# Performance work log

Measured on AMD Instinct MI355X. Metric: run time of the kernel, lower is better.

The kernel has to match this reference:

```python
import jax, jax.numpy as jnp
import numpy as np

NEG_BIG = -9e15  # matches torch's -9000000000000000.0 mask value
ALPHA = 0.2      # LeakyReLU negative slope


def setup_inputs() -> dict:
    key = jax.random.key(0)
    k1, k2, k3 = jax.random.split(key, 3)
    B, N, Fin, Fout = 8, 2048, 64, 64
    h = jax.random.normal(k1, (B, N, Fin), dtype=jnp.float32)
    adj = jax.random.randint(k2, (B, N, N), 0, 2, dtype=jnp.int32)
    kW, ka = jax.random.split(k3)
    # xavier_uniform with gain=1.414
    gW = 1.414 * np.sqrt(6.0 / (Fin + Fout))
    W = jax.random.uniform(kW, (Fin, Fout), minval=-gW, maxval=gW, dtype=jnp.float32)
    ga = 1.414 * np.sqrt(6.0 / (2 * Fout + 1))
    a = jax.random.uniform(ka, (2 * Fout, 1), minval=-ga, maxval=ga, dtype=jnp.float32)
    return {"h": h, "adj": adj, "W": W, "a": a}


def reference(h, adj, W, a):
    # Wh: [B, N, Fout]
    Wh = jnp.einsum("bnf,fo->bno", h, W)
    Fout = W.shape[1]
    a1 = a[:Fout, 0]   # source part of attention vector
    a2 = a[Fout:, 0]   # target part
    # e_ij = leakyrelu(a1.Wh_i + a2.Wh_j) -- rank-1 decomposition of the
    # repeat/cat construction; avoids the [B,N,N,2F] intermediate.
    s = Wh @ a1        # [B, N]
    t = Wh @ a2        # [B, N]
    e = s[:, :, None] + t[:, None, :]            # [B, N, N]
    e = jnp.where(e > 0, e, ALPHA * e)           # LeakyReLU
    e = jnp.where(adj > 0, e, NEG_BIG)           # adjacency mask
    attention = jax.nn.softmax(e, axis=2)
    # dropout omitted: reference is eval-mode (F.dropout is identity when not training)
    h_prime = jnp.einsum("bij,bjo->bio", attention, Wh)
    return jax.nn.elu(h_prime)                   # concat=True branch
```

## Files before the change

kernel.cpp:

```cpp
#include <hip/hip_runtime.h>


#define ALPHA 0.2f

typedef __attribute__((ext_vector_type(8))) short  short8;
typedef __attribute__((ext_vector_type(4))) float  f32x4;

static __device__ __forceinline__ unsigned short f2bf(float f) {
    unsigned u = __builtin_bit_cast(unsigned, f);
    u += 0x7fffu + ((u >> 16) & 1u);
    return (unsigned short)(u >> 16);
}

static __device__ __forceinline__ unsigned pack_bf2(float lo, float hi) {
    unsigned ulo = __builtin_bit_cast(unsigned, lo) + 0x8000u;
    unsigned uhi = __builtin_bit_cast(unsigned, hi) + 0x8000u;
    return __builtin_amdgcn_perm(uhi, ulo, 0x07060302);
}

__global__ __launch_bounds__(256) void k01(
    const float* __restrict__ h, const int* __restrict__ adj,
    const float* __restrict__ W, const float* __restrict__ a,
    unsigned short* __restrict__ whT, float* __restrict__ sw,
    float* __restrict__ tw, unsigned* __restrict__ mask)
{
    __shared__ float W_l[64 * 65];
    __shared__ float wa[128];
    __shared__ float tile[4 * 16 * 65];

    const int tid = threadIdx.x;

    if (blockIdx.x >= 256) {
        const int mb = blockIdx.x - 256;
        const int4* a4 = (const int4*)adj;
        #pragma unroll 1
        for (int batch = 0; batch < 4; ++batch) {
            const size_t base = (size_t)mb * 8192 + batch * 2048 + tid;
            int4 v[8];
            #pragma unroll
            for (int it = 0; it < 8; ++it) v[it] = a4[base + it * 256];
            #pragma unroll
            for (int it = 0; it < 8; ++it) {
                unsigned nib = (v[it].x != 0 ? 1u : 0u) | (v[it].y != 0 ? 2u : 0u)
                             | (v[it].z != 0 ? 4u : 0u) | (v[it].w != 0 ? 8u : 0u);
                unsigned w = nib << ((tid & 7) * 4);
                w |= __shfl_xor(w, 1, 64);
                w |= __shfl_xor(w, 2, 64);
                w |= __shfl_xor(w, 4, 64);
                if ((tid & 7) == 0) mask[(base + it * 256) >> 3] = w;
            }
        }
        return;
    }

    const int lane = tid & 63, wv = tid >> 6;
    const int im   = lane & 15, kq = lane >> 4;

    #pragma unroll
    for (int k = 0; k < 16; ++k) {
        int e = tid + 256 * k;
        W_l[(e >> 6) * 65 + (e & 63)] = W[e];
    }
    __syncthreads();

    if (tid < 128) {
        int f = tid & 63;
        const float* ap = a + (tid >> 6) * 64;
        float acc = 0.f;
        #pragma unroll 8
        for (int o = 0; o < 64; ++o) acc += W_l[f * 65 + o] * ap[o];
        wa[tid] = acc;
    }
    __syncthreads();

    short8 bf[4][2];
    #pragma unroll
    for (int nb = 0; nb < 4; ++nb)
        #pragma unroll
        for (int ks = 0; ks < 2; ++ks)
            #pragma unroll
            for (int u = 0; u < 8; ++u)
                bf[nb][ks][u] = (short)f2bf(W_l[(ks * 32 + kq * 8 + u) * 65 + nb * 16 + im]);

    const int row0 = blockIdx.x * 64 + wv * 16;
    const int bb = row0 >> 11, n_base = row0 & 2047;
    const float* hrow = h + (size_t)(row0 + im) * 64;

    float hv[2][8];
    short8 af[2];
    float sp = 0.f, tp = 0.f;
    #pragma unroll
    for (int ks = 0; ks < 2; ++ks) {
        float4 A = *(const float4*)(hrow + ks * 32 + kq * 8);
        float4 Bv = *(const float4*)(hrow + ks * 32 + kq * 8 + 4);
        hv[ks][0] = A.x;  hv[ks][1] = A.y;  hv[ks][2] = A.z;  hv[ks][3] = A.w;
        hv[ks][4] = Bv.x; hv[ks][5] = Bv.y; hv[ks][6] = Bv.z; hv[ks][7] = Bv.w;
        #pragma unroll
        for (int u = 0; u < 8; ++u) {
            int f = ks * 32 + kq * 8 + u;
            sp += hv[ks][u] * wa[f];
            tp += hv[ks][u] * wa[64 + f];
            af[ks][u] = (short)f2bf(hv[ks][u]);
        }
    }
    sp += __shfl_xor(sp, 16, 64); sp += __shfl_xor(sp, 32, 64);
    tp += __shfl_xor(tp, 16, 64); tp += __shfl_xor(tp, 32, 64);
    if (lane < 16) {
        sw[row0 + lane] = sp;
        tw[row0 + lane] = tp;
    }

    f32x4 acc[4] = {{0.f,0.f,0.f,0.f},{0.f,0.f,0.f,0.f},{0.f,0.f,0.f,0.f},{0.f,0.f,0.f,0.f}};
    #pragma unroll
    for (int ks = 0; ks < 2; ++ks)
        #pragma unroll
        for (int nb = 0; nb < 4; ++nb)
            acc[nb] = __builtin_amdgcn_mfma_f32_16x16x32_bf16(af[ks], bf[nb][ks], acc[nb], 0, 0, 0);

    #pragma unroll
    for (int nb = 0; nb < 4; ++nb)
        #pragma unroll
        for (int r = 0; r < 4; ++r)
            tile[wv * 1040 + (kq * 4 + r) * 65 + nb * 16 + im] = acc[nb][r];
    __syncthreads();

    #pragma unroll
    for (int k = 0; k < 16; ++k) {
        int o = kq + 4 * k;
        float v = tile[wv * 1040 + im * 65 + o];
        whT[(size_t)(bb * 64 + o) * 2048 + n_base + im] = f2bf(v);
    }
}

__global__ __launch_bounds__(256, 4) void k2_attn(
    const unsigned* __restrict__ mask, const unsigned short* __restrict__ whT,
    const float* __restrict__ sw, const float* __restrict__ tw,
    float* __restrict__ out)
{
    __shared__ float t_l[2048];
    __shared__ float cpart[4 * 1040];
    __shared__ float zp[64];

    const int tid  = threadIdx.x;
    const int lane = tid & 63, wv = tid >> 6;
    const int im   = lane & 15, kq = lane >> 4;
    const int b    = blockIdx.x >> 7;
    const int i0   = (blockIdx.x & 127) << 4;

    {
        const float4* tp4 = (const float4*)(tw + (size_t)b * 2048);
        *(float4*)&t_l[tid * 4]         = tp4[tid];
        *(float4*)&t_l[(tid + 256) * 4] = tp4[tid + 256];
    }

    const unsigned* mrow = mask + (size_t)(b * 2048 + i0 + im) * 64 + wv * 16;
    uint4 m0 = *(const uint4*)mrow,        m1 = *(const uint4*)(mrow + 4);
    uint4 m2 = *(const uint4*)(mrow + 8),  m3 = *(const uint4*)(mrow + 12);
    unsigned mm[16] = {m0.x, m0.y, m0.z, m0.w, m1.x, m1.y, m1.z, m1.w,
                       m2.x, m2.y, m2.z, m2.w, m3.x, m3.y, m3.z, m3.w};

    const float sl = sw[b * 2048 + i0 + im];
    const int j00 = wv * 512 + kq * 8;
    const unsigned short* whp0 = whT + ((size_t)(b * 64 +  0 + im) * 2048 + j00);
    const unsigned short* whp1 = whT + ((size_t)(b * 64 + 16 + im) * 2048 + j00);
    const unsigned short* whp2 = whT + ((size_t)(b * 64 + 32 + im) * 2048 + j00);
    const unsigned short* whp3 = whT + ((size_t)(b * 64 + 48 + im) * 2048 + j00);
    const int tbase = wv * 512 + kq * 8;

    __syncthreads();

    f32x4 acc0 = {0.f,0.f,0.f,0.f}, acc1 = {0.f,0.f,0.f,0.f};
    f32x4 acc2 = {0.f,0.f,0.f,0.f}, acc3 = {0.f,0.f,0.f,0.f};
    float zs = 0.f;

    short8 w0 = *(const short8*)(const void*)whp0;
    short8 w1 = *(const short8*)(const void*)whp1;
    short8 w2 = *(const short8*)(const void*)whp2;
    short8 w3 = *(const short8*)(const void*)whp3;

    #pragma unroll
    for (int s = 0; s < 16; ++s) {
        short8 n0 = w0, n1 = w1, n2 = w2, n3 = w3;
        if (s < 15) {
            n0 = *(const short8*)(const void*)(whp0 + (s + 1) * 32);
            n1 = *(const short8*)(const void*)(whp1 + (s + 1) * 32);
            n2 = *(const short8*)(const void*)(whp2 + (s + 1) * 32);
            n3 = *(const short8*)(const void*)(whp3 + (s + 1) * 32);
        }

        float4 tA = *(const float4*)&t_l[tbase + s * 32];
        float4 tB = *(const float4*)&t_l[tbase + s * 32 + 4];
        const unsigned mbyte = (mm[s] >> (kq * 8)) & 0xffu;

        float tv[8] = {tA.x, tA.y, tA.z, tA.w, tB.x, tB.y, tB.z, tB.w};
        float p[8];
        #pragma unroll
        for (int u = 0; u < 8; ++u) {
            float e = sl + tv[u];
            e = fmaxf(e, ALPHA * e);
            float w = __expf(e);
            p[u] = (mbyte & (1u << u)) ? w : 0.f;
            zs += p[u];
        }

        int4 ai;
        ai.x = (int)pack_bf2(p[0], p[1]);
        ai.y = (int)pack_bf2(p[2], p[3]);
        ai.z = (int)pack_bf2(p[4], p[5]);
        ai.w = (int)pack_bf2(p[6], p[7]);
        short8 af = __builtin_bit_cast(short8, ai);

        acc0 = __builtin_amdgcn_mfma_f32_16x16x32_bf16(af, w0, acc0, 0, 0, 0);
        acc1 = __builtin_amdgcn_mfma_f32_16x16x32_bf16(af, w1, acc1, 0, 0, 0);
        acc2 = __builtin_amdgcn_mfma_f32_16x16x32_bf16(af, w2, acc2, 0, 0, 0);
        acc3 = __builtin_amdgcn_mfma_f32_16x16x32_bf16(af, w3, acc3, 0, 0, 0);

        w0 = n0; w1 = n1; w2 = n2; w3 = n3;
    }

    zs += __shfl_xor(zs, 16, 64);
    zs += __shfl_xor(zs, 32, 64);
    if (lane < 16) zp[wv * 16 + lane] = zs;

    #pragma unroll
    for (int r = 0; r < 4; ++r) {
        cpart[wv * 1040 + (kq * 4 + r) * 65 +  0 + im] = acc0[r];
        cpart[wv * 1040 + (kq * 4 + r) * 65 + 16 + im] = acc1[r];
        cpart[wv * 1040 + (kq * 4 + r) * 65 + 32 + im] = acc2[r];
        cpart[wv * 1040 + (kq * 4 + r) * 65 + 48 + im] = acc3[r];
    }
    __syncthreads();

    #pragma unroll
    for (int k = 0; k < 4; ++k) {
        int idx = tid + 256 * k;
        int i = idx >> 6, o = idx & 63;
        float ssum = cpart[0 * 1040 + i * 65 + o] + cpart[1 * 1040 + i * 65 + o]
                   + cpart[2 * 1040 + i * 65 + o] + cpart[3 * 1040 + i * 65 + o];
        float z = zp[i] + zp[16 + i] + zp[32 + i] + zp[48 + i];
        if (z == 0.f) z = 1.f;
        float r = ssum / z;
        out[((size_t)(b * 2048 + i0 + i)) * 64 + o] = r > 0.f ? r : expm1f(r);
    }
}

extern "C" void kernel_launch(void* const* d_in, const int* in_sizes, int n_in,
                              void* d_out, int out_size, void* d_ws, size_t ws_size,
                              hipStream_t stream) {
    const float* h   = (const float*)d_in[0];
    const int*   adj = (const int*)d_in[1];
    const float* W   = (const float*)d_in[2];
    const float* a   = (const float*)d_in[3];
    float* out = (float*)d_out;

    unsigned short* whT = (unsigned short*)d_ws;
    float* sw  = (float*)((char*)d_ws + 2097152);
    float* tw  = (float*)((char*)d_ws + 2097152 + 65536);
    unsigned* mask = (unsigned*)((char*)d_ws + 2097152 + 131072);

    hipLaunchKernelGGL(k01, dim3(1280), dim3(256), 0, stream, h, adj, W, a, whT, sw, tw, mask);
    hipLaunchKernelGGL(k2_attn, dim3(1024), dim3(256), 0, stream, mask, whT, sw, tw, out);
}
```

Before: 236.1 us.

## Pack adjacency mask per-thread to bytes, drop prefetch, relax k2 launch bounds

The adjacency-to-bitmask pass now has each thread read two int4 vectors and write one mask byte directly. This removes the cross-lane shuffle reduction and the strided word stores. The attention kernel drops its manual software prefetch of the Wh tiles and loads them inside the unrolled loop, leaving scheduling to the compiler. Launch bounds change from 4 to 2 waves per SIMD, which gives more registers but may lower occupancy. The exp calls are made conditional on the mask bit and the row-sum accumulation is written as a reduction tree.

```diff
diff --git a/kernel.cpp b/kernel.cpp
--- a/kernel.cpp
+++ b/kernel.cpp
@@ -22,7 +22,7 @@
     const float* __restrict__ h, const int* __restrict__ adj,
     const float* __restrict__ W, const float* __restrict__ a,
     unsigned short* __restrict__ whT, float* __restrict__ sw,
-    float* __restrict__ tw, unsigned* __restrict__ mask)
+    float* __restrict__ tw, unsigned char* __restrict__ mask)
 {
     __shared__ float W_l[64 * 65];
     __shared__ float wa[128];
@@ -34,21 +34,25 @@
         const int mb = blockIdx.x - 256;
         const int4* a4 = (const int4*)adj;
         #pragma unroll 1
-        for (int batch = 0; batch < 4; ++batch) {
-            const size_t base = (size_t)mb * 8192 + batch * 2048 + tid;
-            int4 v[8];
-            #pragma unroll
-            for (int it = 0; it < 8; ++it) v[it] = a4[base + it * 256];
-            #pragma unroll
-            for (int it = 0; it < 8; ++it) {
-                unsigned nib = (v[it].x != 0 ? 1u : 0u) | (v[it].y != 0 ? 2u : 0u)
-                             | (v[it].z != 0 ? 4u : 0u) | (v[it].w != 0 ? 8u : 0u);
-                unsigned w = nib << ((tid & 7) * 4);
-                w |= __shfl_xor(w, 1, 64);
-                w |= __shfl_xor(w, 2, 64);
-                w |= __shfl_xor(w, 4, 64);
-                if ((tid & 7) == 0) mask[(base + it * 256) >> 3] = w;
-            }
+        for (int g0 = 0; g0 < 16; g0 += 4) {
+            int4 v0a, v0b, v1a, v1b, v2a, v2b, v3a, v3b;
+            const size_t p0 = (size_t)mb * 4096 + (size_t)g0 * 256 + tid;
+            v0a = a4[p0 * 2];          v0b = a4[p0 * 2 + 1];
+            v1a = a4[(p0 + 256) * 2];  v1b = a4[(p0 + 256) * 2 + 1];
+            v2a = a4[(p0 + 512) * 2];  v2b = a4[(p0 + 512) * 2 + 1];
+            v3a = a4[(p0 + 768) * 2];  v3b = a4[(p0 + 768) * 2 + 1];
+            unsigned b0 = (v0a.x ? 1u:0u)|(v0a.y ? 2u:0u)|(v0a.z ? 4u:0u)|(v0a.w ? 8u:0u)
+                        | (v0b.x ?16u:0u)|(v0b.y ?32u:0u)|(v0b.z ?64u:0u)|(v0b.w ?128u:0u);
+            unsigned b1 = (v1a.x ? 1u:0u)|(v1a.y ? 2u:0u)|(v1a.z ? 4u:0u)|(v1a.w ? 8u:0u)
+                        | (v1b.x ?16u:0u)|(v1b.y ?32u:0u)|(v1b.z ?64u:0u)|(v1b.w ?128u:0u);
+            unsigned b2 = (v2a.x ? 1u:0u)|(v2a.y ? 2u:0u)|(v2a.z ? 4u:0u)|(v2a.w ? 8u:0u)
+                        | (v2b.x ?16u:0u)|(v2b.y ?32u:0u)|(v2b.z ?64u:0u)|(v2b.w ?128u:0u);
+            unsigned b3 = (v3a.x ? 1u:0u)|(v3a.y ? 2u:0u)|(v3a.z ? 4u:0u)|(v3a.w ? 8u:0u)
+                        | (v3b.x ?16u:0u)|(v3b.y ?32u:0u)|(v3b.z ?64u:0u)|(v3b.w ?128u:0u);
+            mask[p0]       = (unsigned char)b0;
+            mask[p0 + 256] = (unsigned char)b1;
+            mask[p0 + 512] = (unsigned char)b2;
+            mask[p0 + 768] = (unsigned char)b3;
         }
         return;
     }
@@ -132,7 +136,7 @@
     }
 }
 
-__global__ __launch_bounds__(256, 4) void k2_attn(
+__global__ __launch_bounds__(256, 2) void k2_attn(
     const unsigned* __restrict__ mask, const unsigned short* __restrict__ whT,
     const float* __restrict__ sw, const float* __restrict__ tw,
     float* __restrict__ out)
@@ -153,11 +157,10 @@
         *(float4*)&t_l[(tid + 256) * 4] = tp4[tid + 256];
     }
 
-    const unsigned* mrow = mask + (size_t)(b * 2048 + i0 + im) * 64 + wv * 16;
-    uint4 m0 = *(const uint4*)mrow,        m1 = *(const uint4*)(mrow + 4);
-    uint4 m2 = *(const uint4*)(mrow + 8),  m3 = *(const uint4*)(mrow + 12);
-    unsigned mm[16] = {m0.x, m0.y, m0.z, m0.w, m1.x, m1.y, m1.z, m1.w,
-                       m2.x, m2.y, m2.z, m2.w, m3.x, m3.y, m3.z, m3.w};
+    const uint4* mrow4 = (const uint4*)(mask + (size_t)(b * 2048 + i0 + im) * 64 + wv * 16);
+    const uint4 mA = mrow4[0], mB = mrow4[1], mC = mrow4[2], mD = mrow4[3];
+    const unsigned mm[16] = {mA.x, mA.y, mA.z, mA.w, mB.x, mB.y, mB.z, mB.w,
+                             mC.x, mC.y, mC.z, mC.w, mD.x, mD.y, mD.z, mD.w};
 
     const float sl = sw[b * 2048 + i0 + im];
     const int j00 = wv * 512 + kq * 8;
@@ -165,7 +168,6 @@
     const unsigned short* whp1 = whT + ((size_t)(b * 64 + 16 + im) * 2048 + j00);
     const unsigned short* whp2 = whT + ((size_t)(b * 64 + 32 + im) * 2048 + j00);
     const unsigned short* whp3 = whT + ((size_t)(b * 64 + 48 + im) * 2048 + j00);
-    const int tbase = wv * 512 + kq * 8;
 
     __syncthreads();
 
@@ -173,49 +175,48 @@
     f32x4 acc2 = {0.f,0.f,0.f,0.f}, acc3 = {0.f,0.f,0.f,0.f};
     float zs = 0.f;
 
-    short8 w0 = *(const short8*)(const void*)whp0;
-    short8 w1 = *(const short8*)(const void*)whp1;
-    short8 w2 = *(const short8*)(const void*)whp2;
-    short8 w3 = *(const short8*)(const void*)whp3;
-
     #pragma unroll
     for (int s = 0; s < 16; ++s) {
-        short8 n0 = w0, n1 = w1, n2 = w2, n3 = w3;
-        if (s < 15) {
-            n0 = *(const short8*)(const void*)(whp0 + (s + 1) * 32);
-            n1 = *(const short8*)(const void*)(whp1 + (s + 1) * 32);
-            n2 = *(const short8*)(const void*)(whp2 + (s + 1) * 32);
-            n3 = *(const short8*)(const void*)(whp3 + (s + 1) * 32);
-        }
-
-        float4 tA = *(const float4*)&t_l[tbase + s * 32];
-        float4 tB = *(const float4*)&t_l[tbase + s * 32 + 4];
+        const short8 w0 = *(const short8*)(const void*)(whp0 + s * 32);
+        const short8 w1 = *(const short8*)(const void*)(whp1 + s * 32);
+        const short8 w2 = *(const short8*)(const void*)(whp2 + s * 32);
+        const short8 w3 = *(const short8*)(const void*)(whp3 + s * 32);
+
+        const float4 tA = *(const float4*)&t_l[j00 + s * 32];
+        const float4 tB = *(const float4*)&t_l[j00 + s * 32 + 4];
         const unsigned mbyte = (mm[s] >> (kq * 8)) & 0xffu;
 
-        float tv[8] = {tA.x, tA.y, tA.z, tA.w, tB.x, tB.y, tB.z, tB.w};
-        float p[8];
-        #pragma unroll
-        for (int u = 0; u < 8; ++u) {
-            float e = sl + tv[u];
-            e = fmaxf(e, ALPHA * e);
-            float w = __expf(e);
-            p[u] = (mbyte & (1u << u)) ? w : 0.f;
-            zs += p[u];
-        }
+        float e0 = sl + tA.x; e0 = fmaxf(e0, ALPHA * e0);
+        float e1 = sl + tA.y; e1 = fmaxf(e1, ALPHA * e1);
+        float e2 = sl + tA.z; e2 = fmaxf(e2, ALPHA * e2);
+        float e3 = sl + tA.w; e3 = fmaxf(e3, ALPHA * e3);
+        float e4 = sl + tB.x; e4 = fmaxf(e4, ALPHA * e4);
+        float e5 = sl + tB.y; e5 = fmaxf(e5, ALPHA * e5);
+        float e6 = sl + tB.z; e6 = fmaxf(e6, ALPHA * e6);
+        float e7 = sl + tB.w; e7 = fmaxf(e7, ALPHA * e7);
+
+        float p0 = (mbyte &   1u) ? __expf(e0) : 0.f;
+        float p1 = (mbyte &   2u) ? __expf(e1) : 0.f;
+        float p2 = (mbyte &   4u) ? __expf(e2) : 0.f;
+        float p3 = (mbyte &   8u) ? __expf(e3) : 0.f;
+        float p4 = (mbyte &  16u) ? __expf(e4) : 0.f;
+        float p5 = (mbyte &  32u) ? __expf(e5) : 0.f;
+        float p6 = (mbyte &  64u) ? __expf(e6) : 0.f;
+        float p7 = (mbyte & 128u) ? __expf(e7) : 0.f;
+
+        zs += ((p0 + p1) + (p2 + p3)) + ((p4 + p5) + (p6 + p7));
 
         int4 ai;
-        ai.x = (int)pack_bf2(p[0], p[1]);
-        ai.y = (int)pack_bf2(p[2], p[3]);
-        ai.z = (int)pack_bf2(p[4], p[5]);
-        ai.w = (int)pack_bf2(p[6], p[7]);
-        short8 af = __builtin_bit_cast(short8, ai);
+        ai.x = (int)pack_bf2(p0, p1);
+        ai.y = (int)pack_bf2(p2, p3);
+        ai.z = (int)pack_bf2(p4, p5);
+        ai.w = (int)pack_bf2(p6, p7);
+        const short8 af = __builtin_bit_cast(short8, ai);
 
         acc0 = __builtin_amdgcn_mfma_f32_16x16x32_bf16(af, w0, acc0, 0, 0, 0);
         acc1 = __builtin_amdgcn_mfma_f32_16x16x32_bf16(af, w1, acc1, 0, 0, 0);
         acc2 = __builtin_amdgcn_mfma_f32_16x16x32_bf16(af, w2, acc2, 0, 0, 0);
         acc3 = __builtin_amdgcn_mfma_f32_16x16x32_bf16(af, w3, acc3, 0, 0, 0);
-
-        w0 = n0; w1 = n1; w2 = n2; w3 = n3;
     }
 
     zs += __shfl_xor(zs, 16, 64);
@@ -256,8 +257,9 @@
     unsigned short* whT = (unsigned short*)d_ws;
     float* sw  = (float*)((char*)d_ws + 2097152);
     float* tw  = (float*)((char*)d_ws + 2097152 + 65536);
-    unsigned* mask = (unsigned*)((char*)d_ws + 2097152 + 131072);
+    unsigned char* mask = (unsigned char*)((char*)d_ws + 2097152 + 131072);
 
     hipLaunchKernelGGL(k01, dim3(1280), dim3(256), 0, stream, h, adj, W, a, whT, sw, tw, mask);
-    hipLaunchKernelGGL(k2_attn, dim3(1024), dim3(256), 0, stream, mask, whT, sw, tw, out);
-}
+    hipLaunchKernelGGL(k2_attn, dim3(1024), dim3(256), 0, stream,
+                       (const unsigned*)mask, whT, sw, tw, out);
+}
```

Result: no change. 233.0 us (-1.3%).
